# Optimization experiments

Hardware: AMD Instinct MI355X
Metric: run time of the kernel (lower is better)

Reference implementation:

```python
import jax, jax.numpy as jnp
import numpy as np

NEG_SLOPE = 0.01  # nn.LeakyReLU default
N_NODES = 38332
POI_LEN = 38333
CAT_LEN = 400
POI_DIM = 300
CAT_DIM = 100
GCN_CH = 64
GCN_LAYERS = 5
N_EDGES = N_NODES * 32


def leaky(x):
    return jnp.where(x >= 0, x, NEG_SLOPE * x)


def gcn_conv(x, src, dst, W, b):
    """PyG GCNConv: add self loops + symmetric normalization.
    out = D^-1/2 (A+I) D^-1/2 X W + b, deg computed with self loops."""
    n = x.shape[0]
    h = x @ W  # [N, out]
    deg = jax.ops.segment_sum(jnp.ones_like(dst, dtype=h.dtype), dst, num_segments=n) + 1.0
    dinv = jax.lax.rsqrt(deg)  # deg >= 1 always (self loop)
    norm = dinv[src] * dinv[dst]  # [E]
    agg = jax.ops.segment_sum(h[src] * norm[:, None], dst, num_segments=n)
    agg = agg + h * (1.0 / deg)[:, None]  # self-loop term: norm_ii = 1/deg_i
    return agg + b


def setup_inputs() -> dict:
    key = jax.random.key(0)
    ks = jax.random.split(key, 16)
    poi_ids = jax.random.randint(ks[0], (N_NODES, 1), 0, POI_LEN).astype(jnp.float32)
    cat_ids = jax.random.randint(ks[1], (N_NODES, 1), 0, CAT_LEN).astype(jnp.float32)
    feats = jax.random.normal(ks[2], (N_NODES, 3), dtype=jnp.float32)
    x = jnp.concatenate([poi_ids, cat_ids, feats], axis=1)  # [N,5]
    edge_index = jax.random.randint(ks[3], (2, N_EDGES), 0, N_NODES, dtype=jnp.int32)

    def glorot(k, shape):
        lim = float(np.sqrt(6.0 / (shape[0] + shape[1])))
        return jax.random.uniform(k, shape, jnp.float32, -lim, lim)

    d_in = POI_DIM + CAT_DIM + 3  # 403
    params = {
        "poi_emb": jax.random.normal(ks[4], (POI_LEN, POI_DIM), jnp.float32),
        "cat_emb": jax.random.normal(ks[5], (CAT_LEN, CAT_DIM), jnp.float32),
        "W_in": glorot(ks[6], (d_in, GCN_CH)),
        "b_in": jnp.zeros((GCN_CH,), jnp.float32),
        "gcn_Ws": jnp.stack([glorot(jax.random.fold_in(ks[7], i), (GCN_CH, GCN_CH)) for i in range(GCN_LAYERS)]),
        "gcn_bs": jnp.zeros((GCN_LAYERS, GCN_CH), jnp.float32),
        "W_out": glorot(ks[8], (GCN_CH, 1)),
        "b_out": jnp.zeros((1,), jnp.float32),
        "fc1_W": glorot(ks[9], (N_NODES, 128)),
        "fc1_b": jnp.zeros((128,), jnp.float32),
        "fc2_W": glorot(ks[10], (128, POI_LEN)),
        "fc2_b": jnpos if False else jnp.zeros((POI_LEN,), jnp.float32),
    }
    return {"x": x, "edge_index": edge_index, **params}


def reference(x, edge_index, poi_emb, cat_emb, W_in, b_in, gcn_Ws, gcn_bs, W_out, b_out, fc1_W, fc1_b, fc2_W, fc2_b):
    src, dst = edge_index[0], edge_index[1]
    poi_f = poi_emb[x[:, 0].astype(jnp.int32)]  # [N,300]
    cat_f = cat_emb[x[:, 1].astype(jnp.int32)]  # [N,100]
    feat = jnp.concatenate([poi_f, cat_f, x[:, 2:5]], axis=1)  # [N,403]
    feat = leaky(gcn_conv(feat, src, dst, W_in, b_in))
    for i in range(GCN_LAYERS):
        t = gcn_conv(feat, src, dst, gcn_Ws[i], gcn_bs[i])
        feat = leaky(t) + t  # GcnUnit: relu(temp) + temp
    feat = leaky(gcn_conv(feat, src, dst, W_out, b_out)).reshape(-1)  # [N]
    h = jax.nn.relu(feat @ fc1_W + fc1_b)
    out = jax.nn.relu(h @ fc2_W + fc2_b)  # [poi_len]
    return out
```

## Files before the change

### kernel.cpp

```cpp
#include <hip/hip_runtime.h>
#include <hip/hip_bf16.h>

#define N_NODES 38332
#define POI_LEN 38333
#define CAT_LEN 400
#define POI_DIM 300
#define CAT_DIM 100
#define N_EDGES (N_NODES * 32)
#define NEG_SLOPE 0.01f
#define B1 ((N_NODES + 127) / 128)
#define SPLIT_CHUNK 4096
#define NSPLIT ((N_EDGES + SPLIT_CHUNK - 1) / SPLIT_CHUNK)
#define PLACE_CAP 8192
#define BCAP 8192

typedef __attribute__((ext_vector_type(8))) short short8;
typedef __attribute__((ext_vector_type(4))) float f32x4;

__device__ __forceinline__ unsigned short f2bf(float f) {
  unsigned u = __float_as_uint(f);
  u += 0x7fff + ((u >> 16) & 1);
  return (unsigned short)(u >> 16);
}
__device__ __forceinline__ float bflo(unsigned u) {
  return __uint_as_float(u << 16);
}
__device__ __forceinline__ float bfhi(unsigned u) {
  return __uint_as_float(u & 0xffff0000u);
}


__global__ void k_zero(int* __restrict__ bcnt, float* __restrict__ h128) {
  int i = blockIdx.x * 256 + threadIdx.x;
  if (i < B1) bcnt[i] = 0;
  if (i < 128) h128[i] = 0.f;
}

__global__ __launch_bounds__(256) void k_split(const int* __restrict__ src,
                                               const int* __restrict__ dst,
                                               int* __restrict__ bcnt,
                                               int2* __restrict__ staging) {
  __shared__ int hist[B1];
  __shared__ int lbase[B1];
  __shared__ int lcur[B1];
  int tid = threadIdx.x;
  int base = blockIdx.x * SPLIT_CHUNK;
  int n = N_EDGES - base;
  if (n > SPLIT_CHUNK) n = SPLIT_CHUNK;
  for (int b = tid; b < B1; b += 256) {
    hist[b] = 0;
    lcur[b] = 0;
  }
  __syncthreads();
  for (int i = tid; i < n; i += 256) atomicAdd(&hist[dst[base + i] >> 7], 1);
  __syncthreads();
  for (int b = tid; b < B1; b += 256) {
    int c = hist[b];
    lbase[b] = c ? atomicAdd(&bcnt[b], c) : 0;
  }
  __syncthreads();
  for (int i = tid; i < n; i += 256) {
    int d = dst[base + i];
    int s = src[base + i];
    int b = d >> 7;
    int off = atomicAdd(&lcur[b], 1);
    staging[(size_t)b * BCAP + lbase[b] + off] = make_int2(s, d);
  }
}

__global__ __launch_bounds__(256) void k_bscan(const int* __restrict__ bcnt,
                                               int* __restrict__ bbase) {
  __shared__ int sb[256];
  __shared__ int s_tot;
  int tid = threadIdx.x;
  int running = 0;
  for (int b0 = 0; b0 < B1; b0 += 256) {
    int i = b0 + tid;
    int v = (i < B1) ? bcnt[i] : 0;
    sb[tid] = v;
    __syncthreads();
    for (int off = 1; off < 256; off <<= 1) {
      int t = (tid >= off) ? sb[tid - off] : 0;
      __syncthreads();
      sb[tid] += t;
      __syncthreads();
    }
    if (i < B1) bbase[i] = running + sb[tid] - v;
    if (tid == 255) s_tot = sb[255];
    __syncthreads();
    running += s_tot;
  }
  if (tid == 0) bbase[B1] = running;
}

__global__ __launch_bounds__(256) void k_place(const int2* __restrict__ staging,
                                               const int* __restrict__ bcnt,
                                               const int* __restrict__ bbase,
                                               int* __restrict__ csr_src,
                                               int* __restrict__ row_start,
                                               float* __restrict__ dinv) {
  __shared__ int lc[128];
  __shared__ int ls[256];
  __shared__ int cur[128];
  __shared__ int buf[PLACE_CAP];
  int b = blockIdx.x;
  int tid = threadIdx.x;
  int d0 = b * 128;
  int nd = N_NODES - d0;
  if (nd > 128) nd = 128;
  int cnt_b = bcnt[b];
  int base = bbase[b];
  const int2* st = staging + (size_t)b * BCAP;
  if (tid < 128) lc[tid] = 0;
  __syncthreads();
  for (int i = tid; i < cnt_b; i += 256) atomicAdd(&lc[st[i].y - d0], 1);
  __syncthreads();
  int v = (tid < 128) ? lc[tid] : 0;
  ls[tid] = v;
  __syncthreads();
  for (int off = 1; off < 128; off <<= 1) {
    int t = (tid >= off) ? ls[tid - off] : 0;
    __syncthreads();
    ls[tid] += t;
    __syncthreads();
  }
  if (tid < 128) {
    int excl = ls[tid] - v;
    cur[tid] = excl;
    if (tid < nd) {
      row_start[d0 + tid] = base + excl;
      dinv[d0 + tid] = 1.0f / sqrtf((float)(v + 1));
    }
  }
  if (b == B1 - 1 && tid == 0) row_start[N_NODES] = base + cnt_b;
  __syncthreads();
  for (int i = tid; i < cnt_b; i += 256) {
    int2 p = st[i];
    int pos = atomicAdd(&cur[p.y - d0], 1);
    buf[pos] = p.x;
  }
  __syncthreads();
  for (int i = tid; i < cnt_b; i += 256) csr_src[base + i] = buf[i];
}


__global__ void k_wswz(const float* __restrict__ W, int K, int total,
                       unsigned short* __restrict__ Wf) {
  int idx = blockIdx.x * 256 + threadIdx.x;
  if (idx >= total) return;
  int j = idx & 7;
  int n = (idx >> 3) & 63;
  int q = (idx >> 9) & 3;
  int ks = idx >> 11;
  int k = ks * 32 + q * 8 + j;
  float v = (k < K) ? W[k * 64 + n] : 0.f;
  Wf[idx] = f2bf(v);
}


template <int EPI, int K, int K_pad>
__global__ __launch_bounds__(256) void k_projm(const float* __restrict__ A,
                                               const unsigned short* __restrict__ Wf,
                                               void* __restrict__ Cout, int M,
                                               const float* __restrict__ dinv) {
  constexpr int RS = K_pad + 8;
  __shared__ unsigned short sA[16 * RS];
  __shared__ float sC[16 * 68];
  int tid = threadIdx.x;
  int lane = tid & 63;
  int wv = tid >> 6;
  int row0 = blockIdx.x * 16;

  constexpr int NKP4 = K_pad / 4;
  for (int idx = tid; idx < 16 * NKP4; idx += 256) {
    int r = idx / NKP4;
    int k = (idx - r * NKP4) * 4;
    int row = row0 + r;
    ushort4 o = {0, 0, 0, 0};
    if (row < M && k < K) {
      float4 f = *(const float4*)(A + (size_t)row * K + k);
      o.x = f2bf(f.x); o.y = f2bf(f.y); o.z = f2bf(f.z); o.w = f2bf(f.w);
    }
    *(ushort4*)&sA[r * RS + k] = o;
  }
  __syncthreads();

  int c = lane & 15;
  int q = lane >> 4;
  int n0 = wv * 16;
  f32x4 acc = {0.f, 0.f, 0.f, 0.f};
  const unsigned short* arow = &sA[c * RS];
#pragma unroll
  for (int ks = 0; ks < K_pad / 32; ks++) {
    short8 af = *(const short8*)(arow + ks * 32 + q * 8);
    short8 bf = *(const short8*)(Wf + ((size_t)((ks * 4 + q) * 64 + n0 + c)) * 8);
    acc = __builtin_amdgcn_mfma_f32_16x16x32_bf16(af, bf, acc, 0, 0, 0);
  }
#pragma unroll
  for (int r = 0; r < 4; r++) sC[(q * 4 + r) * 68 + n0 + c] = acc[r];
  __syncthreads();

  for (int idx = tid; idx < 16 * 64; idx += 256) {
    int r = idx >> 6, col = idx & 63;
    int row = row0 + r;
    if (row < M) {
      float v = sC[r * 68 + col];
      if (EPI == 0) {
        ((float*)Cout)[(size_t)row * 64 + col] = v;
      } else {
        ((unsigned short*)Cout)[(size_t)row * 64 + col] = f2bf(v * dinv[row]);
      }
    }
  }
}


__global__ __launch_bounds__(256) void k_gather(
    const float* __restrict__ x, const float* __restrict__ proj_poi,
    const float* __restrict__ proj_cat, const float* __restrict__ W_in,
    const float* __restrict__ dinv, unsigned short* __restrict__ hs) {
  int lane = threadIdx.x & 63;
  int w = threadIdx.x >> 6;
  int node = blockIdx.x * 4 + w;
  int pid = (int)x[node * 5 + 0];
  int cid = (int)x[node * 5 + 1];
  float x2 = x[node * 5 + 2];
  float x3 = x[node * 5 + 3];
  float x4 = x[node * 5 + 4];
  float v = proj_poi[(size_t)pid * 64 + lane] + proj_cat[(size_t)cid * 64 + lane] +
            x2 * W_in[400 * 64 + lane] + x3 * W_in[401 * 64 + lane] +
            x4 * W_in[402 * 64 + lane];
  hs[(size_t)node * 64 + lane] = f2bf(v * dinv[node]);
}


template <int MODE>
__global__ __launch_bounds__(256) void k_agg(const unsigned short* __restrict__ hs,
                                             const int* __restrict__ row_start,
                                             const int* __restrict__ csr_src,
                                             const float* __restrict__ dinv,
                                             const float* __restrict__ bias,
                                             float* __restrict__ feat) {
  int tid = threadIdx.x;
  int lane = tid & 63;
  int wv = tid >> 6;
  int node = blockIdx.x * 4 + wv;
  int eslot = lane >> 3;
  int ch8 = lane & 7;
  int r0 = row_start[node];
  int r1 = row_start[node + 1];
  float4 a0 = {0.f, 0.f, 0.f, 0.f}, a1 = a0, b0 = a0, b1 = a0;
  int e = r0 + eslot;
  for (; e + 8 < r1; e += 16) {
    int s0 = csr_src[e];
    int s1 = csr_src[e + 8];
    uint4 v0 = *(const uint4*)(hs + (size_t)s0 * 64 + ch8 * 8);
    uint4 v1 = *(const uint4*)(hs + (size_t)s1 * 64 + ch8 * 8);
    a0.x += bflo(v0.x); a0.y += bfhi(v0.x); a0.z += bflo(v0.y); a0.w += bfhi(v0.y);
    a1.x += bflo(v0.z); a1.y += bfhi(v0.z); a1.z += bflo(v0.w); a1.w += bfhi(v0.w);
    b0.x += bflo(v1.x); b0.y += bfhi(v1.x); b0.z += bflo(v1.y); b0.w += bfhi(v1.y);
    b1.x += bflo(v1.z); b1.y += bfhi(v1.z); b1.z += bflo(v1.w); b1.w += bfhi(v1.w);
  }
  if (e < r1) {
    int s = csr_src[e];
    uint4 v = *(const uint4*)(hs + (size_t)s * 64 + ch8 * 8);
    a0.x += bflo(v.x); a0.y += bfhi(v.x); a0.z += bflo(v.y); a0.w += bfhi(v.y);
    a1.x += bflo(v.z); a1.y += bfhi(v.z); a1.z += bflo(v.w); a1.w += bfhi(v.w);
  }
  float4 v0, v1;
  v0.x = a0.x + b0.x; v0.y = a0.y + b0.y; v0.z = a0.z + b0.z; v0.w = a0.w + b0.w;
  v1.x = a1.x + b1.x; v1.y = a1.y + b1.y; v1.z = a1.z + b1.z; v1.w = a1.w + b1.w;
#pragma unroll
  for (int off = 8; off <= 32; off <<= 1) {
    v0.x += __shfl_xor(v0.x, off, 64);
    v0.y += __shfl_xor(v0.y, off, 64);
    v0.z += __shfl_xor(v0.z, off, 64);
    v0.w += __shfl_xor(v0.w, off, 64);
    v1.x += __shfl_xor(v1.x, off, 64);
    v1.y += __shfl_xor(v1.y, off, 64);
    v1.z += __shfl_xor(v1.z, off, 64);
    v1.w += __shfl_xor(v1.w, off, 64);
  }
  if (lane < 8) {
    uint4 sv = *(const uint4*)(hs + (size_t)node * 64 + ch8 * 8);
    float4 bb0 = *(const float4*)(bias + ch8 * 8);
    float4 bb1 = *(const float4*)(bias + ch8 * 8 + 4);
    float dn = dinv[node];
    float4 t0, t1, o0, o1;
    t0.x = dn * (v0.x + bflo(sv.x)) + bb0.x;
    t0.y = dn * (v0.y + bfhi(sv.x)) + bb0.y;
    t0.z = dn * (v0.z + bflo(sv.y)) + bb0.z;
    t0.w = dn * (v0.w + bfhi(sv.y)) + bb0.w;
    t1.x = dn * (v1.x + bflo(sv.z)) + bb1.x;
    t1.y = dn * (v1.y + bfhi(sv.z)) + bb1.y;
    t1.z = dn * (v1.z + bflo(sv.w)) + bb1.z;
    t1.w = dn * (v1.w + bfhi(sv.w)) + bb1.w;
    float4 l0, l1;
    l0.x = (t0.x >= 0.f) ? t0.x : NEG_SLOPE * t0.x;
    l0.y = (t0.y >= 0.f) ? t0.y : NEG_SLOPE * t0.y;
    l0.z = (t0.z >= 0.f) ? t0.z : NEG_SLOPE * t0.z;
    l0.w = (t0.w >= 0.f) ? t0.w : NEG_SLOPE * t0.w;
    l1.x = (t1.x >= 0.f) ? t1.x : NEG_SLOPE * t1.x;
    l1.y = (t1.y >= 0.f) ? t1.y : NEG_SLOPE * t1.y;
    l1.z = (t1.z >= 0.f) ? t1.z : NEG_SLOPE * t1.z;
    l1.w = (t1.w >= 0.f) ? t1.w : NEG_SLOPE * t1.w;
    if (MODE) {
      o0.x = l0.x + t0.x; o0.y = l0.y + t0.y; o0.z = l0.z + t0.z; o0.w = l0.w + t0.w;
      o1.x = l1.x + t1.x; o1.y = l1.y + t1.y; o1.z = l1.z + t1.z; o1.w = l1.w + t1.w;
    } else {
      o0 = l0; o1 = l1;
    }
    *(float4*)(feat + (size_t)node * 64 + ch8 * 8) = o0;
    *(float4*)(feat + (size_t)node * 64 + ch8 * 8 + 4) = o1;
  }
}


__global__ __launch_bounds__(256) void k_out_xform(const float* __restrict__ feat,
                                                   const float* __restrict__ W_out,
                                                   const float* __restrict__ dinv,
                                                   float* __restrict__ hs1) {
  int lane = threadIdx.x & 63;
  int w = threadIdx.x >> 6;
  int node = blockIdx.x * 4 + w;
  float v = feat[(size_t)node * 64 + lane] * W_out[lane];
#pragma unroll
  for (int off = 32; off; off >>= 1) v += __shfl_xor(v, off, 64);
  if (lane == 0) hs1[node] = v * dinv[node];
}

__global__ __launch_bounds__(256) void k_out_agg(const float* __restrict__ hs1,
                                                 const int* __restrict__ row_start,
                                                 const int* __restrict__ csr_src,
                                                 const float* __restrict__ dinv,
                                                 const float* __restrict__ b_out,
                                                 float* __restrict__ g) {
  int lane = threadIdx.x & 63;
  int w = threadIdx.x >> 6;
  int node = blockIdx.x * 4 + w;
  int r0 = row_start[node];
  int r1 = row_start[node + 1];
  float acc = 0.f;
  for (int e = r0 + lane; e < r1; e += 64) acc += hs1[csr_src[e]];
#pragma unroll
  for (int off = 32; off; off >>= 1) acc += __shfl_xor(acc, off, 64);
  if (lane == 0) {
    float t = dinv[node] * (acc + hs1[node]) + b_out[0];
    g[node] = (t >= 0.f) ? t : NEG_SLOPE * t;
  }
}


__global__ __launch_bounds__(128) void k_fc1(const float* __restrict__ g,
                                             const float* __restrict__ fc1_W,
                                             float* __restrict__ h128) {
  int j = threadIdx.x;
  int base = blockIdx.x * 32;
  int end = base + 32;
  if (end > N_NODES) end = N_NODES;
  float acc = 0.f;
  int i = base;
  for (; i + 4 <= end; i += 4) {
    acc += g[i + 0] * fc1_W[(size_t)(i + 0) * 128 + j];
    acc += g[i + 1] * fc1_W[(size_t)(i + 1) * 128 + j];
    acc += g[i + 2] * fc1_W[(size_t)(i + 2) * 128 + j];
    acc += g[i + 3] * fc1_W[(size_t)(i + 3) * 128 + j];
  }
  for (; i < end; i++) acc += g[i] * fc1_W[(size_t)i * 128 + j];
  atomicAdd(&h128[j], acc);
}

__global__ __launch_bounds__(256) void k_fc2(const float* __restrict__ h128raw,
                                             const float* __restrict__ fc1_b,
                                             const float* __restrict__ fc2_W,
                                             const float* __restrict__ fc2_b,
                                             float* __restrict__ out) {
  __shared__ float sh[128];
  int tid = threadIdx.x;
  if (tid < 128) {
    float v = h128raw[tid] + fc1_b[tid];
    sh[tid] = (v > 0.f) ? v : 0.f;
  }
  __syncthreads();
  int p = blockIdx.x * 256 + tid;
  if (p < POI_LEN) {
    float acc = fc2_b[p];
#pragma unroll 8
    for (int j = 0; j < 128; j++) acc += sh[j] * fc2_W[(size_t)j * POI_LEN + p];
    out[p] = (acc > 0.f) ? acc : 0.f;
  }
}


extern "C" void kernel_launch(void* const* d_in, const int* in_sizes, int n_in,
                              void* d_out, int out_size, void* d_ws, size_t ws_size,
                              hipStream_t stream) {
  const float* x       = (const float*)d_in[0];
  const int*   ei      = (const int*)d_in[1];
  const float* poi_emb = (const float*)d_in[2];
  const float* cat_emb = (const float*)d_in[3];
  const float* W_in    = (const float*)d_in[4];
  const float* b_in    = (const float*)d_in[5];
  const float* gcn_Ws  = (const float*)d_in[6];
  const float* gcn_bs  = (const float*)d_in[7];
  const float* W_out   = (const float*)d_in[8];
  const float* b_out   = (const float*)d_in[9];
  const float* fc1_W   = (const float*)d_in[10];
  const float* fc1_b   = (const float*)d_in[11];
  const float* fc2_W   = (const float*)d_in[12];
  const float* fc2_b   = (const float*)d_in[13];
  const int* src = ei;
  const int* dst = ei + N_EDGES;

  char* p = (char*)d_ws;
  auto take = [&](size_t bytes) {
    char* r = p;
    p += (bytes + 255) & ~(size_t)255;
    return r;
  };
  int*   row_start = (int*)take((size_t)(N_NODES + 1) * 4);
  float* dinv      = (float*)take((size_t)N_NODES * 4);
  int*   bcnt      = (int*)take((size_t)B1 * 4);
  int*   bbase     = (int*)take((size_t)(B1 + 1) * 4);
  int*   csr_src   = (int*)take((size_t)N_EDGES * 4);
  float* feat      = (float*)take((size_t)N_NODES * 64 * 4);
  unsigned short* hs = (unsigned short*)take((size_t)N_NODES * 64 * 2);
  float* proj_poi  = (float*)take((size_t)POI_LEN * 64 * 4);
  float* proj_cat  = (float*)take((size_t)CAT_LEN * 64 * 4);
  float* hs1       = (float*)take((size_t)N_NODES * 4);
  float* g         = (float*)take((size_t)N_NODES * 4);
  float* h128      = (float*)take(128 * 4);
  unsigned short* wf_poi = (unsigned short*)take((size_t)320 * 64 * 2);
  unsigned short* wf_cat = (unsigned short*)take((size_t)128 * 64 * 2);
  unsigned short* wf_gcn = (unsigned short*)take((size_t)5 * 64 * 64 * 2);
  int2* staging = (int2*)feat;
  float* out = (float*)d_out;

  const int nb4 = N_NODES / 4;
  const int nb16 = (N_NODES + 15) / 16;

  k_zero<<<2, 256, 0, stream>>>(bcnt, h128);
  k_split<<<NSPLIT, 256, 0, stream>>>(src, dst, bcnt, staging);
  k_bscan<<<1, 256, 0, stream>>>(bcnt, bbase);
  k_place<<<B1, 256, 0, stream>>>(staging, bcnt, bbase, csr_src, row_start, dinv);

  k_wswz<<<(320 * 64 + 255) / 256, 256, 0, stream>>>(W_in, POI_DIM, 320 * 64, wf_poi);
  k_wswz<<<(128 * 64 + 255) / 256, 256, 0, stream>>>(W_in + 300 * 64, CAT_DIM,
                                                     128 * 64, wf_cat);
  for (int l = 0; l < 5; l++)
    k_wswz<<<(64 * 64 + 255) / 256, 256, 0, stream>>>(
        gcn_Ws + (size_t)l * 64 * 64, 64, 64 * 64, wf_gcn + (size_t)l * 64 * 64);

  k_projm<0, POI_DIM, 320><<<(POI_LEN + 15) / 16, 256, 0, stream>>>(
      poi_emb, wf_poi, proj_poi, POI_LEN, nullptr);
  k_projm<0, CAT_DIM, 128><<<(CAT_LEN + 15) / 16, 256, 0, stream>>>(
      cat_emb, wf_cat, proj_cat, CAT_LEN, nullptr);
  k_gather<<<nb4, 256, 0, stream>>>(x, proj_poi, proj_cat, W_in, dinv, hs);

  k_agg<0><<<nb4, 256, 0, stream>>>(hs, row_start, csr_src, dinv, b_in, feat);
  for (int l = 0; l < 5; l++) {
    k_projm<1, 64, 64><<<nb16, 256, 0, stream>>>(
        feat, wf_gcn + (size_t)l * 64 * 64, hs, N_NODES, dinv);
    k_agg<1><<<nb4, 256, 0, stream>>>(hs, row_start, csr_src, dinv,
                                      gcn_bs + (size_t)l * 64, feat);
  }

  k_out_xform<<<nb4, 256, 0, stream>>>(feat, W_out, dinv, hs1);
  k_out_agg<<<nb4, 256, 0, stream>>>(hs1, row_start, csr_src, dinv, b_out, g);
  k_fc1<<<(N_NODES + 31) / 32, 128, 0, stream>>>(g, fc1_W, h128);
  k_fc2<<<(POI_LEN + 255) / 256, 256, 0, stream>>>(h128, fc1_b, fc2_W, fc2_b, out);
}
```

Measured before the change: 465.7 us.

## Fuse front-end gather with input projection, pack staging, drop scan, bf16 features

Several changes land at once. Weight swizzles and zeroing are merged into one prep kernel, and the bucket scan is removed by giving each bucket a fixed CSR region, with row start and count stored as an int2. Staging entries are packed into a single int. The embedding projection over all POI rows is replaced by a per-node gather-then-MFMA front kernel, so only the rows that nodes actually use are projected. Intermediate features are stored as bf16 instead of f32, the aggregation loop is unrolled four edges deep, and the output transform is fused into the last aggregation. The cost is extra rounding from bf16 features and a padded CSR array.

```diff
diff --git a/kernel.cpp b/kernel.cpp
--- a/kernel.cpp
+++ b/kernel.cpp
@@ -30,16 +30,36 @@
 }
 
 
-__global__ void k_zero(int* __restrict__ bcnt, float* __restrict__ h128) {
-  int i = blockIdx.x * 256 + threadIdx.x;
-  if (i < B1) bcnt[i] = 0;
-  if (i < 128) h128[i] = 0.f;
-}
+#define WFIN_ELEMS (13 * 2048)
+#define WFGCN_ELEMS (5 * 4096)
+
+__global__ __launch_bounds__(256) void k_prep(const float* __restrict__ W_in,
+                                              const float* __restrict__ gcn_Ws,
+                                              unsigned short* __restrict__ wf_in,
+                                              unsigned short* __restrict__ wf_gcn,
+                                              int* __restrict__ bcnt,
+                                              float* __restrict__ h128) {
+  int idx = blockIdx.x * 256 + threadIdx.x;
+  if (idx < B1) bcnt[idx] = 0;
+  if (idx < 128) h128[idx] = 0.f;
+  if (idx < WFIN_ELEMS) {
+    int j = idx & 7, n = (idx >> 3) & 63, q = (idx >> 9) & 3, ks = idx >> 11;
+    int k = ks * 32 + q * 8 + j;
+    wf_in[idx] = f2bf((k < 400) ? W_in[k * 64 + n] : 0.f);
+  } else if (idx < WFIN_ELEMS + WFGCN_ELEMS) {
+    int t = idx - WFIN_ELEMS;
+    int l = t >> 12, i = t & 4095;
+    int j = i & 7, n = (i >> 3) & 63, q = (i >> 9) & 3, ks = i >> 11;
+    int k = ks * 32 + q * 8 + j;
+    wf_gcn[t] = f2bf(gcn_Ws[(size_t)l * 4096 + k * 64 + n]);
+  }
+}
+
 
 __global__ __launch_bounds__(256) void k_split(const int* __restrict__ src,
                                                const int* __restrict__ dst,
                                                int* __restrict__ bcnt,
-                                               int2* __restrict__ staging) {
+                                               int* __restrict__ staging) {
   __shared__ int hist[B1];
   __shared__ int lbase[B1];
   __shared__ int lcur[B1];
@@ -64,40 +84,14 @@
     int s = src[base + i];
     int b = d >> 7;
     int off = atomicAdd(&lcur[b], 1);
-    staging[(size_t)b * BCAP + lbase[b] + off] = make_int2(s, d);
-  }
-}
-
-__global__ __launch_bounds__(256) void k_bscan(const int* __restrict__ bcnt,
-                                               int* __restrict__ bbase) {
-  __shared__ int sb[256];
-  __shared__ int s_tot;
-  int tid = threadIdx.x;
-  int running = 0;
-  for (int b0 = 0; b0 < B1; b0 += 256) {
-    int i = b0 + tid;
-    int v = (i < B1) ? bcnt[i] : 0;
-    sb[tid] = v;
-    __syncthreads();
-    for (int off = 1; off < 256; off <<= 1) {
-      int t = (tid >= off) ? sb[tid - off] : 0;
-      __syncthreads();
-      sb[tid] += t;
-      __syncthreads();
-    }
-    if (i < B1) bbase[i] = running + sb[tid] - v;
-    if (tid == 255) s_tot = sb[255];
-    __syncthreads();
-    running += s_tot;
-  }
-  if (tid == 0) bbase[B1] = running;
-}
-
-__global__ __launch_bounds__(256) void k_place(const int2* __restrict__ staging,
+    staging[(size_t)b * BCAP + lbase[b] + off] = (s << 7) | (d & 127);
+  }
+}
+
+__global__ __launch_bounds__(256) void k_place(const int* __restrict__ staging,
                                                const int* __restrict__ bcnt,
-                                               const int* __restrict__ bbase,
                                                int* __restrict__ csr_src,
-                                               int* __restrict__ row_start,
+                                               int2* __restrict__ rs,
                                                float* __restrict__ dinv) {
   __shared__ int lc[128];
   __shared__ int ls[256];
@@ -109,11 +103,10 @@
   int nd = N_NODES - d0;
   if (nd > 128) nd = 128;
   int cnt_b = bcnt[b];
-  int base = bbase[b];
-  const int2* st = staging + (size_t)b * BCAP;
+  const int* st = staging + (size_t)b * BCAP;
   if (tid < 128) lc[tid] = 0;
   __syncthreads();
-  for (int i = tid; i < cnt_b; i += 256) atomicAdd(&lc[st[i].y - d0], 1);
+  for (int i = tid; i < cnt_b; i += 256) atomicAdd(&lc[st[i] & 127], 1);
   __syncthreads();
   int v = (tid < 128) ? lc[tid] : 0;
   ls[tid] = v;
@@ -128,70 +121,109 @@
     int excl = ls[tid] - v;
     cur[tid] = excl;
     if (tid < nd) {
-      row_start[d0 + tid] = base + excl;
+      rs[d0 + tid] = make_int2(b * BCAP + excl, v);
       dinv[d0 + tid] = 1.0f / sqrtf((float)(v + 1));
     }
   }
-  if (b == B1 - 1 && tid == 0) row_start[N_NODES] = base + cnt_b;
   __syncthreads();
   for (int i = tid; i < cnt_b; i += 256) {
-    int2 p = st[i];
-    int pos = atomicAdd(&cur[p.y - d0], 1);
-    buf[pos] = p.x;
-  }
-  __syncthreads();
+    int p = st[i];
+    int pos = atomicAdd(&cur[p & 127], 1);
+    buf[pos] = p >> 7;
+  }
+  __syncthreads();
+  int base = b * BCAP;
   for (int i = tid; i < cnt_b; i += 256) csr_src[base + i] = buf[i];
 }
 
 
-__global__ void k_wswz(const float* __restrict__ W, int K, int total,
-                       unsigned short* __restrict__ Wf) {
-  int idx = blockIdx.x * 256 + threadIdx.x;
-  if (idx >= total) return;
-  int j = idx & 7;
-  int n = (idx >> 3) & 63;
-  int q = (idx >> 9) & 3;
-  int ks = idx >> 11;
-  int k = ks * 32 + q * 8 + j;
-  float v = (k < K) ? W[k * 64 + n] : 0.f;
-  Wf[idx] = f2bf(v);
-}
-
-
-template <int EPI, int K, int K_pad>
-__global__ __launch_bounds__(256) void k_projm(const float* __restrict__ A,
-                                               const unsigned short* __restrict__ Wf,
-                                               void* __restrict__ Cout, int M,
-                                               const float* __restrict__ dinv) {
-  constexpr int RS = K_pad + 8;
+__global__ __launch_bounds__(256) void k_front(
+    const float* __restrict__ x, const float* __restrict__ poi_emb,
+    const float* __restrict__ cat_emb, const float* __restrict__ W_in,
+    const unsigned short* __restrict__ wf_in, const float* __restrict__ dinv,
+    unsigned short* __restrict__ hs) {
+  constexpr int KP = 416, RS = 424, NK4 = 104;
   __shared__ unsigned short sA[16 * RS];
   __shared__ float sC[16 * 68];
-  int tid = threadIdx.x;
-  int lane = tid & 63;
-  int wv = tid >> 6;
+  __shared__ int sPid[16], sCid[16];
+  __shared__ float sX[16][3];
+  int tid = threadIdx.x;
   int row0 = blockIdx.x * 16;
-
-  constexpr int NKP4 = K_pad / 4;
-  for (int idx = tid; idx < 16 * NKP4; idx += 256) {
-    int r = idx / NKP4;
-    int k = (idx - r * NKP4) * 4;
+  if (tid < 16) {
+    int row = row0 + tid;
+    if (row < N_NODES) {
+      sPid[tid] = (int)x[row * 5 + 0];
+      sCid[tid] = (int)x[row * 5 + 1];
+      sX[tid][0] = x[row * 5 + 2];
+      sX[tid][1] = x[row * 5 + 3];
+      sX[tid][2] = x[row * 5 + 4];
+    } else {
+      sPid[tid] = 0; sCid[tid] = 0;
+      sX[tid][0] = sX[tid][1] = sX[tid][2] = 0.f;
+    }
+  }
+  __syncthreads();
+  for (int idx = tid; idx < 16 * NK4; idx += 256) {
+    int r = idx / NK4;
+    int k = (idx - r * NK4) * 4;
+    ushort4 o = {0, 0, 0, 0};
+    if (k < 400 && row0 + r < N_NODES) {
+      float4 f;
+      if (k < 300) f = *(const float4*)(poi_emb + (size_t)sPid[r] * 300 + k);
+      else         f = *(const float4*)(cat_emb + (size_t)sCid[r] * 100 + (k - 300));
+      o.x = f2bf(f.x); o.y = f2bf(f.y); o.z = f2bf(f.z); o.w = f2bf(f.w);
+    }
+    *(ushort4*)&sA[r * RS + k] = o;
+  }
+  __syncthreads();
+  int lane = tid & 63, wv = tid >> 6;
+  int c = lane & 15, q = lane >> 4, n0 = wv * 16;
+  f32x4 acc = {0.f, 0.f, 0.f, 0.f};
+  const unsigned short* arow = &sA[c * RS];
+#pragma unroll
+  for (int ks = 0; ks < KP / 32; ks++) {
+    short8 af = *(const short8*)(arow + ks * 32 + q * 8);
+    short8 bf = *(const short8*)(wf_in + ((size_t)((ks * 4 + q) * 64 + n0 + c)) * 8);
+    acc = __builtin_amdgcn_mfma_f32_16x16x32_bf16(af, bf, acc, 0, 0, 0);
+  }
+#pragma unroll
+  for (int r = 0; r < 4; r++) sC[(q * 4 + r) * 68 + n0 + c] = acc[r];
+  __syncthreads();
+  for (int idx = tid; idx < 16 * 64; idx += 256) {
+    int r = idx >> 6, col = idx & 63;
+    int row = row0 + r;
+    if (row < N_NODES) {
+      float v = sC[r * 68 + col] + sX[r][0] * W_in[400 * 64 + col] +
+                sX[r][1] * W_in[401 * 64 + col] + sX[r][2] * W_in[402 * 64 + col];
+      hs[(size_t)row * 64 + col] = f2bf(v * dinv[row]);
+    }
+  }
+}
+
+
+__global__ __launch_bounds__(256) void k_projg(const unsigned short* __restrict__ A,
+                                               const unsigned short* __restrict__ Wf,
+                                               unsigned short* __restrict__ hs,
+                                               const float* __restrict__ dinv) {
+  constexpr int RS = 72;
+  __shared__ unsigned short sA[16 * RS];
+  __shared__ float sC[16 * 68];
+  int tid = threadIdx.x;
+  int row0 = blockIdx.x * 16;
+  {
+    int r = tid >> 4, k4 = (tid & 15) * 4;
     int row = row0 + r;
     ushort4 o = {0, 0, 0, 0};
-    if (row < M && k < K) {
-      float4 f = *(const float4*)(A + (size_t)row * K + k);
-      o.x = f2bf(f.x); o.y = f2bf(f.y); o.z = f2bf(f.z); o.w = f2bf(f.w);
-    }
-    *(ushort4*)&sA[r * RS + k] = o;
-  }
-  __syncthreads();
-
-  int c = lane & 15;
-  int q = lane >> 4;
-  int n0 = wv * 16;
+    if (row < N_NODES) o = *(const ushort4*)(A + (size_t)row * 64 + k4);
+    *(ushort4*)&sA[r * RS + k4] = o;
+  }
+  __syncthreads();
+  int lane = tid & 63, wv = tid >> 6;
+  int c = lane & 15, q = lane >> 4, n0 = wv * 16;
   f32x4 acc = {0.f, 0.f, 0.f, 0.f};
   const unsigned short* arow = &sA[c * RS];
 #pragma unroll
-  for (int ks = 0; ks < K_pad / 32; ks++) {
+  for (int ks = 0; ks < 2; ks++) {
     short8 af = *(const short8*)(arow + ks * 32 + q * 8);
     short8 bf = *(const short8*)(Wf + ((size_t)((ks * 4 + q) * 64 + n0 + c)) * 8);
     acc = __builtin_amdgcn_mfma_f32_16x16x32_bf16(af, bf, acc, 0, 0, 0);
@@ -199,103 +231,91 @@
 #pragma unroll
   for (int r = 0; r < 4; r++) sC[(q * 4 + r) * 68 + n0 + c] = acc[r];
   __syncthreads();
-
   for (int idx = tid; idx < 16 * 64; idx += 256) {
     int r = idx >> 6, col = idx & 63;
     int row = row0 + r;
-    if (row < M) {
-      float v = sC[r * 68 + col];
-      if (EPI == 0) {
-        ((float*)Cout)[(size_t)row * 64 + col] = v;
-      } else {
-        ((unsigned short*)Cout)[(size_t)row * 64 + col] = f2bf(v * dinv[row]);
-      }
-    }
-  }
-}
-
-
-__global__ __launch_bounds__(256) void k_gather(
-    const float* __restrict__ x, const float* __restrict__ proj_poi,
-    const float* __restrict__ proj_cat, const float* __restrict__ W_in,
-    const float* __restrict__ dinv, unsigned short* __restrict__ hs) {
-  int lane = threadIdx.x & 63;
-  int w = threadIdx.x >> 6;
-  int node = blockIdx.x * 4 + w;
-  int pid = (int)x[node * 5 + 0];
-  int cid = (int)x[node * 5 + 1];
-  float x2 = x[node * 5 + 2];
-  float x3 = x[node * 5 + 3];
-  float x4 = x[node * 5 + 4];
-  float v = proj_poi[(size_t)pid * 64 + lane] + proj_cat[(size_t)cid * 64 + lane] +
-            x2 * W_in[400 * 64 + lane] + x3 * W_in[401 * 64 + lane] +
-            x4 * W_in[402 * 64 + lane];
-  hs[(size_t)node * 64 + lane] = f2bf(v * dinv[node]);
+    if (row < N_NODES) hs[(size_t)row * 64 + col] = f2bf(sC[r * 68 + col] * dinv[row]);
+  }
 }
 
 
 template <int MODE>
 __global__ __launch_bounds__(256) void k_agg(const unsigned short* __restrict__ hs,
-                                             const int* __restrict__ row_start,
+                                             const int2* __restrict__ rs,
                                              const int* __restrict__ csr_src,
                                              const float* __restrict__ dinv,
                                              const float* __restrict__ bias,
-                                             float* __restrict__ feat) {
+                                             unsigned short* __restrict__ feat,
+                                             const float* __restrict__ W_out,
+                                             float* __restrict__ hs1) {
   int tid = threadIdx.x;
   int lane = tid & 63;
   int wv = tid >> 6;
   int node = blockIdx.x * 4 + wv;
   int eslot = lane >> 3;
   int ch8 = lane & 7;
-  int r0 = row_start[node];
-  int r1 = row_start[node + 1];
-  float4 a0 = {0.f, 0.f, 0.f, 0.f}, a1 = a0, b0 = a0, b1 = a0;
+  int2 rr = rs[node];
+  int r0 = rr.x, r1 = rr.x + rr.y;
+  float4 a0 = {0.f, 0.f, 0.f, 0.f}, a1 = a0;
+#define ACC8(v)                                                              \
+  do {                                                                       \
+    a0.x += bflo((v).x); a0.y += bfhi((v).x);                                \
+    a0.z += bflo((v).y); a0.w += bfhi((v).y);                                \
+    a1.x += bflo((v).z); a1.y += bfhi((v).z);                                \
+    a1.z += bflo((v).w); a1.w += bfhi((v).w);                                \
+  } while (0)
   int e = r0 + eslot;
-  for (; e + 8 < r1; e += 16) {
+  for (; e + 24 < r1; e += 32) {
+    int s0 = csr_src[e];
+    int s1 = csr_src[e + 8];
+    int s2 = csr_src[e + 16];
+    int s3 = csr_src[e + 24];
+    uint4 v0 = *(const uint4*)(hs + (size_t)s0 * 64 + ch8 * 8);
+    uint4 v1 = *(const uint4*)(hs + (size_t)s1 * 64 + ch8 * 8);
+    uint4 v2 = *(const uint4*)(hs + (size_t)s2 * 64 + ch8 * 8);
+    uint4 v3 = *(const uint4*)(hs + (size_t)s3 * 64 + ch8 * 8);
+    ACC8(v0); ACC8(v1); ACC8(v2); ACC8(v3);
+  }
+  if (e + 8 < r1) {
     int s0 = csr_src[e];
     int s1 = csr_src[e + 8];
     uint4 v0 = *(const uint4*)(hs + (size_t)s0 * 64 + ch8 * 8);
     uint4 v1 = *(const uint4*)(hs + (size_t)s1 * 64 + ch8 * 8);
-    a0.x += bflo(v0.x); a0.y += bfhi(v0.x); a0.z += bflo(v0.y); a0.w += bfhi(v0.y);
-    a1.x += bflo(v0.z); a1.y += bfhi(v0.z); a1.z += bflo(v0.w); a1.w += bfhi(v0.w);
-    b0.x += bflo(v1.x); b0.y += bfhi(v1.x); b0.z += bflo(v1.y); b0.w += bfhi(v1.y);
-    b1.x += bflo(v1.z); b1.y += bfhi(v1.z); b1.z += bflo(v1.w); b1.w += bfhi(v1.w);
+    ACC8(v0); ACC8(v1);
+    e += 16;
   }
   if (e < r1) {
     int s = csr_src[e];
     uint4 v = *(const uint4*)(hs + (size_t)s * 64 + ch8 * 8);
-    a0.x += bflo(v.x); a0.y += bfhi(v.x); a0.z += bflo(v.y); a0.w += bfhi(v.y);
-    a1.x += bflo(v.z); a1.y += bfhi(v.z); a1.z += bflo(v.w); a1.w += bfhi(v.w);
-  }
-  float4 v0, v1;
-  v0.x = a0.x + b0.x; v0.y = a0.y + b0.y; v0.z = a0.z + b0.z; v0.w = a0.w + b0.w;
-  v1.x = a1.x + b1.x; v1.y = a1.y + b1.y; v1.z = a1.z + b1.z; v1.w = a1.w + b1.w;
+    ACC8(v);
+  }
+#undef ACC8
 #pragma unroll
   for (int off = 8; off <= 32; off <<= 1) {
-    v0.x += __shfl_xor(v0.x, off, 64);
-    v0.y += __shfl_xor(v0.y, off, 64);
-    v0.z += __shfl_xor(v0.z, off, 64);
-    v0.w += __shfl_xor(v0.w, off, 64);
-    v1.x += __shfl_xor(v1.x, off, 64);
-    v1.y += __shfl_xor(v1.y, off, 64);
-    v1.z += __shfl_xor(v1.z, off, 64);
-    v1.w += __shfl_xor(v1.w, off, 64);
+    a0.x += __shfl_xor(a0.x, off, 64);
+    a0.y += __shfl_xor(a0.y, off, 64);
+    a0.z += __shfl_xor(a0.z, off, 64);
+    a0.w += __shfl_xor(a0.w, off, 64);
+    a1.x += __shfl_xor(a1.x, off, 64);
+    a1.y += __shfl_xor(a1.y, off, 64);
+    a1.z += __shfl_xor(a1.z, off, 64);
+    a1.w += __shfl_xor(a1.w, off, 64);
   }
   if (lane < 8) {
     uint4 sv = *(const uint4*)(hs + (size_t)node * 64 + ch8 * 8);
     float4 bb0 = *(const float4*)(bias + ch8 * 8);
     float4 bb1 = *(const float4*)(bias + ch8 * 8 + 4);
     float dn = dinv[node];
-    float4 t0, t1, o0, o1;
-    t0.x = dn * (v0.x + bflo(sv.x)) + bb0.x;
-    t0.y = dn * (v0.y + bfhi(sv.x)) + bb0.y;
-    t0.z = dn * (v0.z + bflo(sv.y)) + bb0.z;
-    t0.w = dn * (v0.w + bfhi(sv.y)) + bb0.w;
-    t1.x = dn * (v1.x + bflo(sv.z)) + bb1.x;
-    t1.y = dn * (v1.y + bfhi(sv.z)) + bb1.y;
-    t1.z = dn * (v1.z + bflo(sv.w)) + bb1.z;
-    t1.w = dn * (v1.w + bfhi(sv.w)) + bb1.w;
-    float4 l0, l1;
+    float4 t0, t1;
+    t0.x = dn * (a0.x + bflo(sv.x)) + bb0.x;
+    t0.y = dn * (a0.y + bfhi(sv.x)) + bb0.y;
+    t0.z = dn * (a0.z + bflo(sv.y)) + bb0.z;
+    t0.w = dn * (a0.w + bfhi(sv.y)) + bb0.w;
+    t1.x = dn * (a1.x + bflo(sv.z)) + bb1.x;
+    t1.y = dn * (a1.y + bfhi(sv.z)) + bb1.y;
+    t1.z = dn * (a1.z + bflo(sv.w)) + bb1.z;
+    t1.w = dn * (a1.w + bfhi(sv.w)) + bb1.w;
+    float4 l0, l1, o0, o1;
     l0.x = (t0.x >= 0.f) ? t0.x : NEG_SLOPE * t0.x;
     l0.y = (t0.y >= 0.f) ? t0.y : NEG_SLOPE * t0.y;
     l0.z = (t0.z >= 0.f) ? t0.z : NEG_SLOPE * t0.z;
@@ -304,33 +324,35 @@
     l1.y = (t1.y >= 0.f) ? t1.y : NEG_SLOPE * t1.y;
     l1.z = (t1.z >= 0.f) ? t1.z : NEG_SLOPE * t1.z;
     l1.w = (t1.w >= 0.f) ? t1.w : NEG_SLOPE * t1.w;
-    if (MODE) {
+    if (MODE == 0) {
+      o0 = l0; o1 = l1;
+    } else {
       o0.x = l0.x + t0.x; o0.y = l0.y + t0.y; o0.z = l0.z + t0.z; o0.w = l0.w + t0.w;
       o1.x = l1.x + t1.x; o1.y = l1.y + t1.y; o1.z = l1.z + t1.z; o1.w = l1.w + t1.w;
+    }
+    if (MODE == 2) {
+      float4 w0 = *(const float4*)(W_out + ch8 * 8);
+      float4 w1 = *(const float4*)(W_out + ch8 * 8 + 4);
+      float p = o0.x * w0.x + o0.y * w0.y + o0.z * w0.z + o0.w * w0.w +
+                o1.x * w1.x + o1.y * w1.y + o1.z * w1.z + o1.w * w1.w;
+      p += __shfl_xor(p, 1, 64);
+      p += __shfl_xor(p, 2, 64);
+      p += __shfl_xor(p, 4, 64);
+      if (lane == 0) hs1[node] = p * dn;
     } else {
-      o0 = l0; o1 = l1;
-    }
-    *(float4*)(feat + (size_t)node * 64 + ch8 * 8) = o0;
-    *(float4*)(feat + (size_t)node * 64 + ch8 * 8 + 4) = o1;
-  }
-}
-
-
-__global__ __launch_bounds__(256) void k_out_xform(const float* __restrict__ feat,
-                                                   const float* __restrict__ W_out,
-                                                   const float* __restrict__ dinv,
-                                                   float* __restrict__ hs1) {
-  int lane = threadIdx.x & 63;
-  int w = threadIdx.x >> 6;
-  int node = blockIdx.x * 4 + w;
-  float v = feat[(size_t)node * 64 + lane] * W_out[lane];
-#pragma unroll
-  for (int off = 32; off; off >>= 1) v += __shfl_xor(v, off, 64);
-  if (lane == 0) hs1[node] = v * dinv[node];
-}
+      uint4 pk;
+      pk.x = (unsigned)f2bf(o0.x) | ((unsigned)f2bf(o0.y) << 16);
+      pk.y = (unsigned)f2bf(o0.z) | ((unsigned)f2bf(o0.w) << 16);
+      pk.z = (unsigned)f2bf(o1.x) | ((unsigned)f2bf(o1.y) << 16);
+      pk.w = (unsigned)f2bf(o1.z) | ((unsigned)f2bf(o1.w) << 16);
+      *(uint4*)(feat + (size_t)node * 64 + ch8 * 8) = pk;
+    }
+  }
+}
+
 
 __global__ __launch_bounds__(256) void k_out_agg(const float* __restrict__ hs1,
-                                                 const int* __restrict__ row_start,
+                                                 const int2* __restrict__ rs,
                                                  const int* __restrict__ csr_src,
                                                  const float* __restrict__ dinv,
                                                  const float* __restrict__ b_out,
@@ -338,8 +360,8 @@
   int lane = threadIdx.x & 63;
   int w = threadIdx.x >> 6;
   int node = blockIdx.x * 4 + w;
-  int r0 = row_start[node];
-  int r1 = row_start[node + 1];
+  int2 rr = rs[node];
+  int r0 = rr.x, r1 = rr.x + rr.y;
   float acc = 0.f;
   for (int e = r0 + lane; e < r1; e += 64) acc += hs1[csr_src[e]];
 #pragma unroll
@@ -418,55 +440,45 @@
     p += (bytes + 255) & ~(size_t)255;
     return r;
   };
-  int*   row_start = (int*)take((size_t)(N_NODES + 1) * 4);
+  int2*  rs        = (int2*)take((size_t)N_NODES * 8);
   float* dinv      = (float*)take((size_t)N_NODES * 4);
   int*   bcnt      = (int*)take((size_t)B1 * 4);
-  int*   bbase     = (int*)take((size_t)(B1 + 1) * 4);
-  int*   csr_src   = (int*)take((size_t)N_EDGES * 4);
-  float* feat      = (float*)take((size_t)N_NODES * 64 * 4);
-  unsigned short* hs = (unsigned short*)take((size_t)N_NODES * 64 * 2);
-  float* proj_poi  = (float*)take((size_t)POI_LEN * 64 * 4);
-  float* proj_cat  = (float*)take((size_t)CAT_LEN * 64 * 4);
+  int*   csr_src   = (int*)take((size_t)B1 * BCAP * 4);
+  unsigned short* feat = (unsigned short*)take((size_t)N_NODES * 64 * 2);
+  unsigned short* hs   = (unsigned short*)take((size_t)N_NODES * 64 * 2);
   float* hs1       = (float*)take((size_t)N_NODES * 4);
   float* g         = (float*)take((size_t)N_NODES * 4);
   float* h128      = (float*)take(128 * 4);
-  unsigned short* wf_poi = (unsigned short*)take((size_t)320 * 64 * 2);
-  unsigned short* wf_cat = (unsigned short*)take((size_t)128 * 64 * 2);
-  unsigned short* wf_gcn = (unsigned short*)take((size_t)5 * 64 * 64 * 2);
-  int2* staging = (int2*)feat;
+  unsigned short* wf_in  = (unsigned short*)take((size_t)WFIN_ELEMS * 2);
+  unsigned short* wf_gcn = (unsigned short*)take((size_t)WFGCN_ELEMS * 2);
+  int* staging = (int*)feat;
   float* out = (float*)d_out;
 
   const int nb4 = N_NODES / 4;
   const int nb16 = (N_NODES + 15) / 16;
 
-  k_zero<<<2, 256, 0, stream>>>(bcnt, h128);
+  k_prep<<<(WFIN_ELEMS + WFGCN_ELEMS + 255) / 256, 256, 0, stream>>>(
+      W_in, gcn_Ws, wf_in, wf_gcn, bcnt, h128);
   k_split<<<NSPLIT, 256, 0, stream>>>(src, dst, bcnt, staging);
-  k_bscan<<<1, 256, 0, stream>>>(bcnt, bbase);
-  k_place<<<B1, 256, 0, stream>>>(staging, bcnt, bbase, csr_src, row_start, dinv);
-
-  k_wswz<<<(320 * 64 + 255) / 256, 256, 0, stream>>>(W_in, POI_DIM, 320 * 64, wf_poi);
-  k_wswz<<<(128 * 64 + 255) / 256, 256, 0, stream>>>(W_in + 300 * 64, CAT_DIM,
-                                                     128 * 64, wf_cat);
-  for (int l = 0; l < 5; l++)
-    k_wswz<<<(64 * 64 + 255) / 256, 256, 0, stream>>>(
-        gcn_Ws + (size_t)l * 64 * 64, 64, 64 * 64, wf_gcn + (size_t)l * 64 * 64);
-
-  k_projm<0, POI_DIM, 320><<<(POI_LEN + 15) / 16, 256, 0, stream>>>(
-      poi_emb, wf_poi, proj_poi, POI_LEN, nullptr);
-  k_projm<0, CAT_DIM, 128><<<(CAT_LEN + 15) / 16, 256, 0, stream>>>(
-      cat_emb, wf_cat, proj_cat, CAT_LEN, nullptr);
-  k_gather<<<nb4, 256, 0, stream>>>(x, proj_poi, proj_cat, W_in, dinv, hs);
-
-  k_agg<0><<<nb4, 256, 0, stream>>>(hs, row_start, csr_src, dinv, b_in, feat);
+  k_place<<<B1, 256, 0, stream>>>(staging, bcnt, csr_src, rs, dinv);
+
+  k_front<<<nb16, 256, 0, stream>>>(x, poi_emb, cat_emb, W_in, wf_in, dinv, hs);
+
+  k_agg<0><<<nb4, 256, 0, stream>>>(hs, rs, csr_src, dinv, b_in, feat, nullptr,
+                                    nullptr);
   for (int l = 0; l < 5; l++) {
-    k_projm<1, 64, 64><<<nb16, 256, 0, stream>>>(
-        feat, wf_gcn + (size_t)l * 64 * 64, hs, N_NODES, dinv);
-    k_agg<1><<<nb4, 256, 0, stream>>>(hs, row_start, csr_src, dinv,
-                                      gcn_bs + (size_t)l * 64, feat);
-  }
-
-  k_out_xform<<<nb4, 256, 0, stream>>>(feat, W_out, dinv, hs1);
-  k_out_agg<<<nb4, 256, 0, stream>>>(hs1, row_start, csr_src, dinv, b_out, g);
+    k_projg<<<nb16, 256, 0, stream>>>(feat, wf_gcn + (size_t)l * 4096, hs, dinv);
+    if (l < 4)
+      k_agg<1><<<nb4, 256, 0, stream>>>(hs, rs, csr_src, dinv,
+                                        gcn_bs + (size_t)l * 64, feat, nullptr,
+                                        nullptr);
+    else
+      k_agg<2><<<nb4, 256, 0, stream>>>(hs, rs, csr_src, dinv,
+                                        gcn_bs + (size_t)l * 64, nullptr, W_out,
+                                        hs1);
+  }
+
+  k_out_agg<<<nb4, 256, 0, stream>>>(hs1, rs, csr_src, dinv, b_out, g);
   k_fc1<<<(N_NODES + 31) / 32, 128, 0, stream>>>(g, fc1_W, h128);
   k_fc2<<<(POI_LEN + 255) / 256, 256, 0, stream>>>(h128, fc1_b, fc2_W, fc2_b, out);
 }
```

Measured after the change: 433.9 us. 1.07x faster.
